# Kernel optimization log

Hardware: AMD Instinct MI355X
Metric: run time of the kernel (lower is better)

## Reference

```python
import jax, jax.numpy as jnp
import numpy as np

B, L, G, D = 4096, 64, 8, 128
N_ITEMS, N_USERS, N_RATINGS = 100000, 50000, 5


def setup_inputs() -> dict:
    key = jax.random.key(0)
    ks = jax.random.split(key, 16)
    s = jnp.float32(0.02)
    return dict(
        nodes=jax.random.randint(ks[0], (B, G), 0, N_USERS),
        history_u=jax.random.randint(ks[1], (B, L), 0, N_ITEMS),
        history_r=jax.random.randint(ks[2], (B, L), 0, N_RATINGS),
        hist_len=jax.random.randint(ks[3], (B,), 0, L),
        v2e_weight=jax.random.normal(ks[4], (N_ITEMS, D), dtype=jnp.float32) * s,
        u2e_weight=jax.random.normal(ks[5], (N_USERS, D), dtype=jnp.float32) * s,
        r2e_weight=jax.random.normal(ks[6], (N_RATINGS, D), dtype=jnp.float32) * s,
        W1=jax.random.normal(ks[7], (2 * D, D), dtype=jnp.float32) * s,
        b1=jnp.zeros((D,), jnp.float32),
        W2=jax.random.normal(ks[8], (D, D), dtype=jnp.float32) * s,
        b2=jnp.zeros((D,), jnp.float32),
        att1_W=jax.random.normal(ks[9], (2 * D, D), dtype=jnp.float32) * s,
        att1_b=jnp.zeros((D,), jnp.float32),
        att2_W=jax.random.normal(ks[10], (D, D), dtype=jnp.float32) * s,
        att2_b=jnp.zeros((D,), jnp.float32),
        att3_W=jax.random.normal(ks[11], (D, 1), dtype=jnp.float32) * s,
        att3_b=jnp.zeros((1,), jnp.float32),
        ge_W=jax.random.normal(ks[12], (D, D), dtype=jnp.float32) * s,
        ge_b=jnp.zeros((D,), jnp.float32),
    )


def reference(nodes, history_u, history_r, hist_len,
              v2e_weight, u2e_weight, r2e_weight,
              W1, b1, W2, b2,
              att1_W, att1_b, att2_W, att2_b, att3_W, att3_b,
              ge_W, ge_b):
    lengths = hist_len + 1                      # ensure >=1 valid history entry per group
    e_uv = v2e_weight[history_u]                # [B, L, D] item-history gather
    e_r = r2e_weight[history_r]                 # [B, L, D] rating gather
    members = u2e_weight[nodes]                 # [B, G, D] member gather
    # Group_Embedding: pool members to one rep per group
    g = jax.nn.relu(members.mean(axis=1) @ ge_W + ge_b)            # [B, D]
    # per-history 2-layer MLP (w_r1, w_r2)
    x = jax.nn.relu(jnp.concatenate([e_uv, e_r], axis=-1) @ W1 + b1)
    o = jax.nn.relu(x @ W2 + b2)                # [B, L, D] o_history
    # Attention: cat(o_history, group_rep) -> relu -> relu -> scalar, softmax over L
    g_rep = jnp.broadcast_to(g[:, None, :], o.shape)               # [B, L, D]
    a = jax.nn.relu(jnp.concatenate([o, g_rep], axis=-1) @ att1_W + att1_b)
    a = jax.nn.relu(a @ att2_W + att2_b)
    logits = (a @ att3_W + att3_b)[..., 0]      # [B, L]
    mask = jnp.arange(L)[None, :] < lengths[:, None]
    logits = jnp.where(mask, logits, jnp.float32(-1e9))
    att = jax.nn.softmax(logits, axis=-1) * mask                   # ragged masked softmax
    # torch.mm(o_history.t(), att_w).t() == attention-weighted reduce over L
    return jnp.einsum('bl,bld->bd', att, o)     # [B, D]
```

## Files before the change

### kernel.cpp

```cpp
#include <hip/hip_runtime.h>
#include <hip/hip_bf16.h>

#define DD 128
#define TILE_BYTES 32768
#define WS_R_OFF   196608
#define WS_GB_OFF  199168

typedef __attribute__((ext_vector_type(8))) short bf16x8;
typedef __attribute__((ext_vector_type(4))) float f32x4;

__device__ inline unsigned short f2bf(float f) {
  unsigned u = __float_as_uint(f);
  return (unsigned short)((u + 0x7fffu + ((u >> 16) & 1u)) >> 16);
}

__device__ inline void async16(void* ldsp, const void* gp) {
  __builtin_amdgcn_global_load_lds(
      (const __attribute__((address_space(1))) void*)gp,
      (__attribute__((address_space(3))) void*)ldsp, 16, 0, 0);
}

__device__ inline void fill_w(char* slot, const char* src, int tid) {
  int w = tid >> 6, lane = tid & 63;
  #pragma unroll
  for (int i = 0; i < 8; ++i) {
    int ofs = ((i << 2) + w) << 10;
    async16(slot + ofs, src + ofs + lane * 16);
  }
}

__device__ inline bf16x8 ldfrag(const char* buf, int rowbase, int kk, int lane) {
  int row = rowbase + (lane & 15);
  int off = (row << 8) + (kk << 6) + (lane & 48);
  off ^= (row & 7) << 4;
  return *(const bf16x8*)(buf + off);
}

__device__ inline bf16x8 ldAg(const float* rp, int kk, int lane) {
  const float4* p = (const float4*)(rp + (kk << 5) + ((lane >> 4) << 3));
  float4 f0 = p[0], f1 = p[1];
  bf16x8 r;
  r[0] = (short)f2bf(f0.x); r[1] = (short)f2bf(f0.y);
  r[2] = (short)f2bf(f0.z); r[3] = (short)f2bf(f0.w);
  r[4] = (short)f2bf(f1.x); r[5] = (short)f2bf(f1.y);
  r[6] = (short)f2bf(f1.z); r[7] = (short)f2bf(f1.w);
  return r;
}

__device__ inline uint2 pack4(float v0, float v1, float v2, float v3) {
  return make_uint2((unsigned)f2bf(v0) | ((unsigned)f2bf(v1) << 16),
                    (unsigned)f2bf(v2) | ((unsigned)f2bf(v3) << 16));
}

#define MFMA(a, b, c) __builtin_amdgcn_mfma_f32_16x16x32_bf16((a), (b), (c), 0, 0, 0)

__global__ __launch_bounds__(256) void prep_weights(
    const float* __restrict__ W1, const float* __restrict__ W2,
    const float* __restrict__ a1W, const float* __restrict__ a2W,
    const float* __restrict__ geW,
    const float* __restrict__ r2e, const float* __restrict__ b1,
    unsigned short* __restrict__ wsw, float* __restrict__ Rp) {
  int gid = blockIdx.x * 256 + threadIdx.x;
  if (gid < 12288) {
    int tile = gid >> 11, idx = gid & 2047;
    int row = idx >> 4, slot = idx & 15;
    int slot2 = slot ^ (row & 7);
    const float* W; int kb;
    switch (tile) {
      case 0:  W = W1;  kb = 0;   break;
      case 1:  W = W2;  kb = 0;   break;
      case 2:  W = a1W; kb = 0;   break;
      case 3:  W = a2W; kb = 0;   break;
      case 4:  W = geW; kb = 0;   break;
      default: W = a1W; kb = 128; break;
    }
    unsigned pk[4];
    #pragma unroll
    for (int p = 0; p < 4; ++p) {
      unsigned short lo = f2bf(W[(size_t)(kb + slot2 * 8 + 2 * p) * DD + row]);
      unsigned short hi = f2bf(W[(size_t)(kb + slot2 * 8 + 2 * p + 1) * DD + row]);
      pk[p] = (unsigned)lo | ((unsigned)hi << 16);
    }
    *(uint4*)(wsw + (size_t)tile * 16384 + (size_t)idx * 8) =
        make_uint4(pk[0], pk[1], pk[2], pk[3]);
  } else {
    int t = gid - 12288;
    for (int idx = t; idx < 640; idx += 256) {
      int r = idx >> 7, d = idx & 127;
      float s = b1[d];
      for (int k = 0; k < 128; ++k)
        s = fmaf(r2e[r * DD + k], W1[(size_t)(DD + k) * DD + d], s);
      Rp[idx] = s;
    }
  }
}

__global__ __launch_bounds__(256, 2) void prep_gb(
    const int* __restrict__ nodes, const float* __restrict__ u2e,
    const float* __restrict__ geb, const float* __restrict__ a1b,
    const char* __restrict__ tiles, float* __restrict__ gbv) {
  __shared__ char mean_s[4096];
  __shared__ char g_s[4096];
  __shared__ char wslot[32768];
  __shared__ int nodes_s[128];
  int tid = threadIdx.x, w = tid >> 6, lane = tid & 63;
  int b0 = blockIdx.x * 16;
  if (tid < 128) nodes_s[tid] = nodes[b0 * 8 + tid];
  fill_w(wslot, tiles + 4 * TILE_BYTES, tid);
  __syncthreads();
  for (int idx = tid; idx < 2048; idx += 256) {
    int row = idx >> 7, d = idx & 127;
    float m = 0.f;
    #pragma unroll
    for (int j = 0; j < 8; ++j)
      m += u2e[(size_t)nodes_s[row * 8 + j] * DD + d];
    m *= 0.125f;
    int off = ((row << 8) + (d << 1)) ^ ((row & 7) << 4);
    *(unsigned short*)(mean_s + off) = f2bf(m);
  }
  __syncthreads();
  int cb = lane & 15, rb = (lane >> 4) << 2;
  f32x4 acc[2] = {(f32x4)(0.f), (f32x4)(0.f)};
  #pragma unroll
  for (int kk = 0; kk < 4; ++kk) {
    bf16x8 a = ldfrag(mean_s, 0, kk, lane);
    #pragma unroll
    for (int nf = 0; nf < 2; ++nf) {
      bf16x8 b = ldfrag(wslot, w * 32 + nf * 16, kk, lane);
      acc[nf] = MFMA(a, b, acc[nf]);
    }
  }
  __syncthreads();
  fill_w(wslot, tiles + 5 * TILE_BYTES, tid);
  #pragma unroll
  for (int nf = 0; nf < 2; ++nf) {
    int col = w * 32 + nf * 16 + cb;
    float gb2 = geb[col];
    #pragma unroll
    for (int j = 0; j < 4; ++j) {
      int row = rb + j;
      float v = fmaxf(acc[nf][j] + gb2, 0.f);
      int off = ((row << 8) + (col << 1)) ^ ((row & 7) << 4);
      *(unsigned short*)(g_s + off) = f2bf(v);
    }
  }
  __syncthreads();
  acc[0] = (f32x4)(0.f); acc[1] = (f32x4)(0.f);
  #pragma unroll
  for (int kk = 0; kk < 4; ++kk) {
    bf16x8 a = ldfrag(g_s, 0, kk, lane);
    #pragma unroll
    for (int nf = 0; nf < 2; ++nf) {
      bf16x8 b = ldfrag(wslot, w * 32 + nf * 16, kk, lane);
      acc[nf] = MFMA(a, b, acc[nf]);
    }
  }
  #pragma unroll
  for (int nf = 0; nf < 2; ++nf) {
    int col = w * 32 + nf * 16 + cb;
    float bb = a1b[col];
    #pragma unroll
    for (int j = 0; j < 4; ++j)
      gbv[(size_t)(b0 + rb + j) * DD + col] = acc[nf][j] + bb;
  }
}

__device__ inline void gemmWX(f32x4 acc[8], const char* Wt, const char* Xt,
                              int mfw, int nlw, int lane) {
  #pragma unroll
  for (int kk = 0; kk < 4; ++kk) {
    bf16x8 bf0 = ldfrag(Xt, nlw * 32, kk, lane);
    bf16x8 bf1 = ldfrag(Xt, nlw * 32 + 16, kk, lane);
    #pragma unroll
    for (int mf = 0; mf < 4; ++mf) {
      bf16x8 a = ldfrag(Wt, mfw * 64 + mf * 16, kk, lane);
      acc[mf * 2]     = MFMA(a, bf0, acc[mf * 2]);
      acc[mf * 2 + 1] = MFMA(a, bf1, acc[mf * 2 + 1]);
    }
  }
}

__global__ __launch_bounds__(256, 3) void main_kernel(
    const int* __restrict__ hu, const int* __restrict__ hr,
    const int* __restrict__ hlen,
    const float* __restrict__ v2e,
    const float* __restrict__ b2, const float* __restrict__ a2b,
    const float* __restrict__ a3W, const float* __restrict__ a3b,
    const char* __restrict__ tiles, const float* __restrict__ Rp,
    const float* __restrict__ gbv, float* __restrict__ out) {
  __shared__ char W[32768];
  __shared__ char X[16384];
  __shared__ float lpart[2][64];
  __shared__ float att_s[64];
  __shared__ float red_s[2][128];

  const int tid = threadIdx.x, lane = tid & 63;
  const int wv = tid >> 6;
  const int mfw = wv >> 1, nlw = wv & 1;
  const int cb = lane & 15, g = lane >> 4;
  const int b0 = blockIdx.x;

  fill_w(W, tiles, tid);
  const int l0 = nlw * 32 + cb, l1 = l0 + 16;
  const int hu0 = hu[b0 * 64 + l0], hu1 = hu[b0 * 64 + l1];
  const int hr0 = hr[b0 * 64 + l0], hr1 = hr[b0 * 64 + l1];
  __syncthreads();

  f32x4 acc[8];
  #pragma unroll
  for (int i = 0; i < 8; ++i) acc[i] = (f32x4)(0.f);

  {
    const float* rp0 = v2e + (size_t)hu0 * DD;
    const float* rp1 = v2e + (size_t)hu1 * DD;
    #pragma unroll
    for (int kk = 0; kk < 4; ++kk) {
      bf16x8 bf0 = ldAg(rp0, kk, lane);
      bf16x8 bf1 = ldAg(rp1, kk, lane);
      #pragma unroll
      for (int mf = 0; mf < 4; ++mf) {
        bf16x8 a = ldfrag(W, mfw * 64 + mf * 16, kk, lane);
        acc[mf * 2]     = MFMA(a, bf0, acc[mf * 2]);
        acc[mf * 2 + 1] = MFMA(a, bf1, acc[mf * 2 + 1]);
      }
    }
  }
  __syncthreads();
  fill_w(W, tiles + TILE_BYTES, tid);
  #pragma unroll
  for (int mf = 0; mf < 4; ++mf) {
    int f0 = mfw * 64 + mf * 16 + g * 4;
    float4 r0 = *(const float4*)(Rp + hr0 * DD + f0);
    float4 r1 = *(const float4*)(Rp + hr1 * DD + f0);
    f32x4 v0 = acc[mf * 2], v1 = acc[mf * 2 + 1];
    uint2 p0 = pack4(fmaxf(v0[0] + r0.x, 0.f), fmaxf(v0[1] + r0.y, 0.f),
                     fmaxf(v0[2] + r0.z, 0.f), fmaxf(v0[3] + r0.w, 0.f));
    uint2 p1 = pack4(fmaxf(v1[0] + r1.x, 0.f), fmaxf(v1[1] + r1.y, 0.f),
                     fmaxf(v1[2] + r1.z, 0.f), fmaxf(v1[3] + r1.w, 0.f));
    int o0 = ((l0 << 8) + (f0 << 1)) ^ ((l0 & 7) << 4);
    int o1 = ((l1 << 8) + (f0 << 1)) ^ ((l1 & 7) << 4);
    *(uint2*)(X + o0) = p0;
    *(uint2*)(X + o1) = p1;
  }
  __syncthreads();

  #pragma unroll
  for (int i = 0; i < 8; ++i) acc[i] = (f32x4)(0.f);
  gemmWX(acc, W, X, mfw, nlw, lane);
  __syncthreads();
  fill_w(W, tiles + 2 * TILE_BYTES, tid);
  uint2 opk[8];
  #pragma unroll
  for (int mf = 0; mf < 4; ++mf) {
    int f0 = mfw * 64 + mf * 16 + g * 4;
    float4 bb = *(const float4*)(b2 + f0);
    f32x4 v0 = acc[mf * 2], v1 = acc[mf * 2 + 1];
    uint2 p0 = pack4(fmaxf(v0[0] + bb.x, 0.f), fmaxf(v0[1] + bb.y, 0.f),
                     fmaxf(v0[2] + bb.z, 0.f), fmaxf(v0[3] + bb.w, 0.f));
    uint2 p1 = pack4(fmaxf(v1[0] + bb.x, 0.f), fmaxf(v1[1] + bb.y, 0.f),
                     fmaxf(v1[2] + bb.z, 0.f), fmaxf(v1[3] + bb.w, 0.f));
    opk[mf * 2] = p0; opk[mf * 2 + 1] = p1;
    int o0 = ((l0 << 8) + (f0 << 1)) ^ ((l0 & 7) << 4);
    int o1 = ((l1 << 8) + (f0 << 1)) ^ ((l1 & 7) << 4);
    *(uint2*)(X + o0) = p0;
    *(uint2*)(X + o1) = p1;
  }
  __syncthreads();

  #pragma unroll
  for (int i = 0; i < 8; ++i) acc[i] = (f32x4)(0.f);
  gemmWX(acc, W, X, mfw, nlw, lane);
  __syncthreads();
  fill_w(W, tiles + 3 * TILE_BYTES, tid);
  #pragma unroll
  for (int mf = 0; mf < 4; ++mf) {
    int f0 = mfw * 64 + mf * 16 + g * 4;
    float4 gg = *(const float4*)(gbv + (size_t)b0 * DD + f0);
    f32x4 v0 = acc[mf * 2], v1 = acc[mf * 2 + 1];
    uint2 p0 = pack4(fmaxf(v0[0] + gg.x, 0.f), fmaxf(v0[1] + gg.y, 0.f),
                     fmaxf(v0[2] + gg.z, 0.f), fmaxf(v0[3] + gg.w, 0.f));
    uint2 p1 = pack4(fmaxf(v1[0] + gg.x, 0.f), fmaxf(v1[1] + gg.y, 0.f),
                     fmaxf(v1[2] + gg.z, 0.f), fmaxf(v1[3] + gg.w, 0.f));
    int o0 = ((l0 << 8) + (f0 << 1)) ^ ((l0 & 7) << 4);
    int o1 = ((l1 << 8) + (f0 << 1)) ^ ((l1 & 7) << 4);
    *(uint2*)(X + o0) = p0;
    *(uint2*)(X + o1) = p1;
  }
  __syncthreads();

  #pragma unroll
  for (int i = 0; i < 8; ++i) acc[i] = (f32x4)(0.f);
  gemmWX(acc, W, X, mfw, nlw, lane);
  {
    float s0 = 0.f, s1 = 0.f;
    #pragma unroll
    for (int mf = 0; mf < 4; ++mf) {
      int f0 = mfw * 64 + mf * 16 + g * 4;
      float4 ab = *(const float4*)(a2b + f0);
      float4 aw = *(const float4*)(a3W + f0);
      f32x4 v0 = acc[mf * 2], v1 = acc[mf * 2 + 1];
      s0 = fmaf(fmaxf(v0[0] + ab.x, 0.f), aw.x, s0);
      s0 = fmaf(fmaxf(v0[1] + ab.y, 0.f), aw.y, s0);
      s0 = fmaf(fmaxf(v0[2] + ab.z, 0.f), aw.z, s0);
      s0 = fmaf(fmaxf(v0[3] + ab.w, 0.f), aw.w, s0);
      s1 = fmaf(fmaxf(v1[0] + ab.x, 0.f), aw.x, s1);
      s1 = fmaf(fmaxf(v1[1] + ab.y, 0.f), aw.y, s1);
      s1 = fmaf(fmaxf(v1[2] + ab.z, 0.f), aw.z, s1);
      s1 = fmaf(fmaxf(v1[3] + ab.w, 0.f), aw.w, s1);
    }
    s0 += __shfl_xor(s0, 16); s0 += __shfl_xor(s0, 32);
    s1 += __shfl_xor(s1, 16); s1 += __shfl_xor(s1, 32);
    if (g == 0) { lpart[mfw][l0] = s0; lpart[mfw][l1] = s1; }
  }
  __syncthreads();

  if (tid < 64) {
    float lv = lpart[0][tid] + lpart[1][tid] + a3b[0];
    int len = hlen[b0] + 1;
    bool valid = tid < len;
    if (!valid) lv = -1e30f;
    float m = lv;
    #pragma unroll
    for (int off = 32; off; off >>= 1) m = fmaxf(m, __shfl_xor(m, off));
    float pe = valid ? expf(lv - m) : 0.f;
    float s = pe;
    #pragma unroll
    for (int off = 32; off; off >>= 1) s += __shfl_xor(s, off);
    att_s[tid] = pe / s;
  }
  __syncthreads();

  {
    float att0 = att_s[l0], att1 = att_s[l1];
    float p[4][4];
    #pragma unroll
    for (int mf = 0; mf < 4; ++mf) {
      uint2 q0 = opk[mf * 2], q1 = opk[mf * 2 + 1];
      p[mf][0] = att0 * __uint_as_float(q0.x << 16)
               + att1 * __uint_as_float(q1.x << 16);
      p[mf][1] = att0 * __uint_as_float(q0.x & 0xffff0000u)
               + att1 * __uint_as_float(q1.x & 0xffff0000u);
      p[mf][2] = att0 * __uint_as_float(q0.y << 16)
               + att1 * __uint_as_float(q1.y << 16);
      p[mf][3] = att0 * __uint_as_float(q0.y & 0xffff0000u)
               + att1 * __uint_as_float(q1.y & 0xffff0000u);
    }
    #pragma unroll
    for (int m = 1; m < 16; m <<= 1) {
      #pragma unroll
      for (int mf = 0; mf < 4; ++mf) {
        p[mf][0] += __shfl_xor(p[mf][0], m);
        p[mf][1] += __shfl_xor(p[mf][1], m);
        p[mf][2] += __shfl_xor(p[mf][2], m);
        p[mf][3] += __shfl_xor(p[mf][3], m);
      }
    }
    if (cb == 0) {
      #pragma unroll
      for (int mf = 0; mf < 4; ++mf) {
        int d = mfw * 64 + mf * 16 + g * 4;
        red_s[nlw][d + 0] = p[mf][0];
        red_s[nlw][d + 1] = p[mf][1];
        red_s[nlw][d + 2] = p[mf][2];
        red_s[nlw][d + 3] = p[mf][3];
      }
    }
  }
  __syncthreads();
  if (tid < 128)
    out[(size_t)b0 * DD + tid] = red_s[0][tid] + red_s[1][tid];
}

extern "C" void kernel_launch(void* const* d_in, const int* in_sizes, int n_in,
                              void* d_out, int out_size, void* d_ws, size_t ws_size,
                              hipStream_t stream) {
  const int*   nodes = (const int*)d_in[0];
  const int*   hu    = (const int*)d_in[1];
  const int*   hr    = (const int*)d_in[2];
  const int*   hlen  = (const int*)d_in[3];
  const float* v2e   = (const float*)d_in[4];
  const float* u2e   = (const float*)d_in[5];
  const float* r2e   = (const float*)d_in[6];
  const float* W1    = (const float*)d_in[7];
  const float* b1    = (const float*)d_in[8];
  const float* W2    = (const float*)d_in[9];
  const float* b2    = (const float*)d_in[10];
  const float* a1W   = (const float*)d_in[11];
  const float* a1b   = (const float*)d_in[12];
  const float* a2W   = (const float*)d_in[13];
  const float* a2b   = (const float*)d_in[14];
  const float* a3W   = (const float*)d_in[15];
  const float* a3b   = (const float*)d_in[16];
  const float* geW   = (const float*)d_in[17];
  const float* geb   = (const float*)d_in[18];
  float* out = (float*)d_out;

  unsigned short* wsw = (unsigned short*)d_ws;
  const char* tiles = (const char*)d_ws;
  float* Rp  = (float*)((char*)d_ws + WS_R_OFF);
  float* gbv = (float*)((char*)d_ws + WS_GB_OFF);

  prep_weights<<<49, 256, 0, stream>>>(W1, W2, a1W, a2W, geW, r2e, b1, wsw, Rp);
  prep_gb<<<256, 256, 0, stream>>>(nodes, u2e, geb, a1b, tiles, gbv);
  main_kernel<<<4096, 256, 0, stream>>>(
      hu, hr, hlen, v2e, b2, a2b, a3W, a3b, tiles, Rp, gbv, out);
}
```

Measured before the change: 111.2 us.

## Make main kernel persistent with resident weights, two rows per iteration

```diff
diff --git a/kernel.cpp b/kernel.cpp
--- a/kernel.cpp
+++ b/kernel.cpp
@@ -180,7 +180,7 @@
   }
 }
 
-__global__ __launch_bounds__(256, 3) void main_kernel(
+__global__ __launch_bounds__(512, 2) void main_kernel(
     const int* __restrict__ hu, const int* __restrict__ hr,
     const int* __restrict__ hlen,
     const float* __restrict__ v2e,
@@ -188,187 +188,262 @@
     const float* __restrict__ a3W, const float* __restrict__ a3b,
     const char* __restrict__ tiles, const float* __restrict__ Rp,
     const float* __restrict__ gbv, float* __restrict__ out) {
-  __shared__ char W[32768];
-  __shared__ char X[16384];
-  __shared__ float lpart[2][64];
-  __shared__ float att_s[64];
-  __shared__ float red_s[2][128];
+  __shared__ char smem[133760];
+  char*  W1s = smem;
+  char*  W2s = smem + 32768;
+  char*  A1s = smem + 65536;
+  char*  XA  = smem + 98304;
+  char*  XB  = smem + 114688;
+  float* Rs  = (float*)(smem + 131072);
 
   const int tid = threadIdx.x, lane = tid & 63;
   const int wv = tid >> 6;
-  const int mfw = wv >> 1, nlw = wv & 1;
+  const int rowsel = wv >> 2;
+  const int w4 = wv & 3;
+  const int mfw = w4 >> 1, nlw = w4 & 1;
   const int cb = lane & 15, g = lane >> 4;
-  const int b0 = blockIdx.x;
-
-  fill_w(W, tiles, tid);
+  char* X = rowsel ? XB : XA;
+
+  #pragma unroll
+  for (int i = 0; i < 4; ++i) {
+    int ofs = (i * 8 + wv) << 10;
+    async16(W1s + ofs, tiles + ofs + lane * 16);
+    async16(W2s + ofs, tiles + TILE_BYTES + ofs + lane * 16);
+    async16(A1s + ofs, tiles + 2 * TILE_BYTES + ofs + lane * 16);
+  }
+  for (int i = tid; i < 640; i += 512)
+    Rs[(i >> 7) * 132 + (i & 127)] = Rp[i];
+
+  bf16x8 a2Wr[16];
+  {
+    const char* a2g = tiles + 3 * TILE_BYTES;
+    #pragma unroll
+    for (int mf = 0; mf < 4; ++mf)
+      #pragma unroll
+      for (int kk = 0; kk < 4; ++kk) {
+        int row = mfw * 64 + mf * 16 + cb;
+        int off = ((row << 8) + (kk << 6) + (lane & 48)) ^ ((row & 7) << 4);
+        a2Wr[mf * 4 + kk] = *(const bf16x8*)(a2g + off);
+      }
+  }
+  float4 a2br[4], a3wr[4];
+  #pragma unroll
+  for (int mf = 0; mf < 4; ++mf) {
+    int f0 = mfw * 64 + mf * 16 + g * 4;
+    a2br[mf] = *(const float4*)(a2b + f0);
+    a3wr[mf] = *(const float4*)(a3W + f0);
+  }
+  const float a3bv = a3b[0];
+
   const int l0 = nlw * 32 + cb, l1 = l0 + 16;
-  const int hu0 = hu[b0 * 64 + l0], hu1 = hu[b0 * 64 + l1];
-  const int hr0 = hr[b0 * 64 + l0], hr1 = hr[b0 * 64 + l1];
+  const int rbase = blockIdx.x * 8;
+  int r = rbase + rowsel;
+  int hu0 = hu[r * 64 + l0], hu1 = hu[r * 64 + l1];
+  int hr0 = hr[r * 64 + l0], hr1 = hr[r * 64 + l1];
   __syncthreads();
 
-  f32x4 acc[8];
-  #pragma unroll
-  for (int i = 0; i < 8; ++i) acc[i] = (f32x4)(0.f);
-
-  {
-    const float* rp0 = v2e + (size_t)hu0 * DD;
-    const float* rp1 = v2e + (size_t)hu1 * DD;
+  for (int p = 0; p < 4; ++p) {
+    f32x4 acc[8];
+    #pragma unroll
+    for (int i = 0; i < 8; ++i) acc[i] = (f32x4)(0.f);
+
+    {
+      const float* rp0 = v2e + (size_t)hu0 * DD;
+      const float* rp1 = v2e + (size_t)hu1 * DD;
+      #pragma unroll
+      for (int kk = 0; kk < 4; ++kk) {
+        bf16x8 bf0 = ldAg(rp0, kk, lane);
+        bf16x8 bf1 = ldAg(rp1, kk, lane);
+        #pragma unroll
+        for (int mf = 0; mf < 4; ++mf) {
+          bf16x8 a = ldfrag(W1s, mfw * 64 + mf * 16, kk, lane);
+          acc[mf * 2]     = MFMA(a, bf0, acc[mf * 2]);
+          acc[mf * 2 + 1] = MFMA(a, bf1, acc[mf * 2 + 1]);
+        }
+      }
+    }
+    #pragma unroll
+    for (int mf = 0; mf < 4; ++mf) {
+      int f0 = mfw * 64 + mf * 16 + g * 4;
+      float4 r0 = *(const float4*)(Rs + hr0 * 132 + f0);
+      float4 r1 = *(const float4*)(Rs + hr1 * 132 + f0);
+      f32x4 v0 = acc[mf * 2], v1 = acc[mf * 2 + 1];
+      uint2 p0 = pack4(fmaxf(v0[0] + r0.x, 0.f), fmaxf(v0[1] + r0.y, 0.f),
+                       fmaxf(v0[2] + r0.z, 0.f), fmaxf(v0[3] + r0.w, 0.f));
+      uint2 p1 = pack4(fmaxf(v1[0] + r1.x, 0.f), fmaxf(v1[1] + r1.y, 0.f),
+                       fmaxf(v1[2] + r1.z, 0.f), fmaxf(v1[3] + r1.w, 0.f));
+      int o0 = ((l0 << 8) + (f0 << 1)) ^ ((l0 & 7) << 4);
+      int o1 = ((l1 << 8) + (f0 << 1)) ^ ((l1 & 7) << 4);
+      *(uint2*)(X + o0) = p0;
+      *(uint2*)(X + o1) = p1;
+    }
+    __syncthreads();
+
+    float4 b2v[4];
+    #pragma unroll
+    for (int mf = 0; mf < 4; ++mf)
+      b2v[mf] = *(const float4*)(b2 + mfw * 64 + mf * 16 + g * 4);
+
+    #pragma unroll
+    for (int i = 0; i < 8; ++i) acc[i] = (f32x4)(0.f);
+    gemmWX(acc, W2s, X, mfw, nlw, lane);
+    __syncthreads();
+    uint2 opk[8];
+    #pragma unroll
+    for (int mf = 0; mf < 4; ++mf) {
+      int f0 = mfw * 64 + mf * 16 + g * 4;
+      float4 bb = b2v[mf];
+      f32x4 v0 = acc[mf * 2], v1 = acc[mf * 2 + 1];
+      uint2 p0 = pack4(fmaxf(v0[0] + bb.x, 0.f), fmaxf(v0[1] + bb.y, 0.f),
+                       fmaxf(v0[2] + bb.z, 0.f), fmaxf(v0[3] + bb.w, 0.f));
+      uint2 p1 = pack4(fmaxf(v1[0] + bb.x, 0.f), fmaxf(v1[1] + bb.y, 0.f),
+                       fmaxf(v1[2] + bb.z, 0.f), fmaxf(v1[3] + bb.w, 0.f));
+      opk[mf * 2] = p0; opk[mf * 2 + 1] = p1;
+      int o0 = ((l0 << 8) + (f0 << 1)) ^ ((l0 & 7) << 4);
+      int o1 = ((l1 << 8) + (f0 << 1)) ^ ((l1 & 7) << 4);
+      *(uint2*)(X + o0) = p0;
+      *(uint2*)(X + o1) = p1;
+    }
+    __syncthreads();
+
+    float4 gg[4];
+    #pragma unroll
+    for (int mf = 0; mf < 4; ++mf)
+      gg[mf] = *(const float4*)(gbv + (size_t)r * DD + mfw * 64 + mf * 16 + g * 4);
+
+    #pragma unroll
+    for (int i = 0; i < 8; ++i) acc[i] = (f32x4)(0.f);
+    gemmWX(acc, A1s, X, mfw, nlw, lane);
+    __syncthreads();
+    #pragma unroll
+    for (int mf = 0; mf < 4; ++mf) {
+      int f0 = mfw * 64 + mf * 16 + g * 4;
+      float4 gv = gg[mf];
+      f32x4 v0 = acc[mf * 2], v1 = acc[mf * 2 + 1];
+      uint2 p0 = pack4(fmaxf(v0[0] + gv.x, 0.f), fmaxf(v0[1] + gv.y, 0.f),
+                       fmaxf(v0[2] + gv.z, 0.f), fmaxf(v0[3] + gv.w, 0.f));
+      uint2 p1 = pack4(fmaxf(v1[0] + gv.x, 0.f), fmaxf(v1[1] + gv.y, 0.f),
+                       fmaxf(v1[2] + gv.z, 0.f), fmaxf(v1[3] + gv.w, 0.f));
+      int o0 = ((l0 << 8) + (f0 << 1)) ^ ((l0 & 7) << 4);
+      int o1 = ((l1 << 8) + (f0 << 1)) ^ ((l1 & 7) << 4);
+      *(uint2*)(X + o0) = p0;
+      *(uint2*)(X + o1) = p1;
+    }
+    __syncthreads();
+
+    int hu0n = 0, hu1n = 0, hr0n = 0, hr1n = 0;
+    if (p < 3) {
+      int rn = r + 2;
+      hu0n = hu[rn * 64 + l0]; hu1n = hu[rn * 64 + l1];
+      hr0n = hr[rn * 64 + l0]; hr1n = hr[rn * 64 + l1];
+    }
+
+    #pragma unroll
+    for (int i = 0; i < 8; ++i) acc[i] = (f32x4)(0.f);
     #pragma unroll
     for (int kk = 0; kk < 4; ++kk) {
-      bf16x8 bf0 = ldAg(rp0, kk, lane);
-      bf16x8 bf1 = ldAg(rp1, kk, lane);
+      bf16x8 bf0 = ldfrag(X, nlw * 32, kk, lane);
+      bf16x8 bf1 = ldfrag(X, nlw * 32 + 16, kk, lane);
       #pragma unroll
       for (int mf = 0; mf < 4; ++mf) {
-        bf16x8 a = ldfrag(W, mfw * 64 + mf * 16, kk, lane);
+        bf16x8 a = a2Wr[mf * 4 + kk];
         acc[mf * 2]     = MFMA(a, bf0, acc[mf * 2]);
         acc[mf * 2 + 1] = MFMA(a, bf1, acc[mf * 2 + 1]);
       }
     }
-  }
-  __syncthreads();
-  fill_w(W, tiles + TILE_BYTES, tid);
-  #pragma unroll
-  for (int mf = 0; mf < 4; ++mf) {
-    int f0 = mfw * 64 + mf * 16 + g * 4;
-    float4 r0 = *(const float4*)(Rp + hr0 * DD + f0);
-    float4 r1 = *(const float4*)(Rp + hr1 * DD + f0);
-    f32x4 v0 = acc[mf * 2], v1 = acc[mf * 2 + 1];
-    uint2 p0 = pack4(fmaxf(v0[0] + r0.x, 0.f), fmaxf(v0[1] + r0.y, 0.f),
-                     fmaxf(v0[2] + r0.z, 0.f), fmaxf(v0[3] + r0.w, 0.f));
-    uint2 p1 = pack4(fmaxf(v1[0] + r1.x, 0.f), fmaxf(v1[1] + r1.y, 0.f),
-                     fmaxf(v1[2] + r1.z, 0.f), fmaxf(v1[3] + r1.w, 0.f));
-    int o0 = ((l0 << 8) + (f0 << 1)) ^ ((l0 & 7) << 4);
-    int o1 = ((l1 << 8) + (f0 << 1)) ^ ((l1 & 7) << 4);
-    *(uint2*)(X + o0) = p0;
-    *(uint2*)(X + o1) = p1;
-  }
-  __syncthreads();
-
-  #pragma unroll
-  for (int i = 0; i < 8; ++i) acc[i] = (f32x4)(0.f);
-  gemmWX(acc, W, X, mfw, nlw, lane);
-  __syncthreads();
-  fill_w(W, tiles + 2 * TILE_BYTES, tid);
-  uint2 opk[8];
-  #pragma unroll
-  for (int mf = 0; mf < 4; ++mf) {
-    int f0 = mfw * 64 + mf * 16 + g * 4;
-    float4 bb = *(const float4*)(b2 + f0);
-    f32x4 v0 = acc[mf * 2], v1 = acc[mf * 2 + 1];
-    uint2 p0 = pack4(fmaxf(v0[0] + bb.x, 0.f), fmaxf(v0[1] + bb.y, 0.f),
-                     fmaxf(v0[2] + bb.z, 0.f), fmaxf(v0[3] + bb.w, 0.f));
-    uint2 p1 = pack4(fmaxf(v1[0] + bb.x, 0.f), fmaxf(v1[1] + bb.y, 0.f),
-                     fmaxf(v1[2] + bb.z, 0.f), fmaxf(v1[3] + bb.w, 0.f));
-    opk[mf * 2] = p0; opk[mf * 2 + 1] = p1;
-    int o0 = ((l0 << 8) + (f0 << 1)) ^ ((l0 & 7) << 4);
-    int o1 = ((l1 << 8) + (f0 << 1)) ^ ((l1 & 7) << 4);
-    *(uint2*)(X + o0) = p0;
-    *(uint2*)(X + o1) = p1;
-  }
-  __syncthreads();
-
-  #pragma unroll
-  for (int i = 0; i < 8; ++i) acc[i] = (f32x4)(0.f);
-  gemmWX(acc, W, X, mfw, nlw, lane);
-  __syncthreads();
-  fill_w(W, tiles + 3 * TILE_BYTES, tid);
-  #pragma unroll
-  for (int mf = 0; mf < 4; ++mf) {
-    int f0 = mfw * 64 + mf * 16 + g * 4;
-    float4 gg = *(const float4*)(gbv + (size_t)b0 * DD + f0);
-    f32x4 v0 = acc[mf * 2], v1 = acc[mf * 2 + 1];
-    uint2 p0 = pack4(fmaxf(v0[0] + gg.x, 0.f), fmaxf(v0[1] + gg.y, 0.f),
-                     fmaxf(v0[2] + gg.z, 0.f), fmaxf(v0[3] + gg.w, 0.f));
-    uint2 p1 = pack4(fmaxf(v1[0] + gg.x, 0.f), fmaxf(v1[1] + gg.y, 0.f),
-                     fmaxf(v1[2] + gg.z, 0.f), fmaxf(v1[3] + gg.w, 0.f));
-    int o0 = ((l0 << 8) + (f0 << 1)) ^ ((l0 & 7) << 4);
-    int o1 = ((l1 << 8) + (f0 << 1)) ^ ((l1 & 7) << 4);
-    *(uint2*)(X + o0) = p0;
-    *(uint2*)(X + o1) = p1;
-  }
-  __syncthreads();
-
-  #pragma unroll
-  for (int i = 0; i < 8; ++i) acc[i] = (f32x4)(0.f);
-  gemmWX(acc, W, X, mfw, nlw, lane);
-  {
-    float s0 = 0.f, s1 = 0.f;
-    #pragma unroll
-    for (int mf = 0; mf < 4; ++mf) {
-      int f0 = mfw * 64 + mf * 16 + g * 4;
-      float4 ab = *(const float4*)(a2b + f0);
-      float4 aw = *(const float4*)(a3W + f0);
-      f32x4 v0 = acc[mf * 2], v1 = acc[mf * 2 + 1];
-      s0 = fmaf(fmaxf(v0[0] + ab.x, 0.f), aw.x, s0);
-      s0 = fmaf(fmaxf(v0[1] + ab.y, 0.f), aw.y, s0);
-      s0 = fmaf(fmaxf(v0[2] + ab.z, 0.f), aw.z, s0);
-      s0 = fmaf(fmaxf(v0[3] + ab.w, 0.f), aw.w, s0);
-      s1 = fmaf(fmaxf(v1[0] + ab.x, 0.f), aw.x, s1);
-      s1 = fmaf(fmaxf(v1[1] + ab.y, 0.f), aw.y, s1);
-      s1 = fmaf(fmaxf(v1[2] + ab.z, 0.f), aw.z, s1);
-      s1 = fmaf(fmaxf(v1[3] + ab.w, 0.f), aw.w, s1);
-    }
-    s0 += __shfl_xor(s0, 16); s0 += __shfl_xor(s0, 32);
-    s1 += __shfl_xor(s1, 16); s1 += __shfl_xor(s1, 32);
-    if (g == 0) { lpart[mfw][l0] = s0; lpart[mfw][l1] = s1; }
-  }
-  __syncthreads();
-
-  if (tid < 64) {
-    float lv = lpart[0][tid] + lpart[1][tid] + a3b[0];
-    int len = hlen[b0] + 1;
-    bool valid = tid < len;
-    if (!valid) lv = -1e30f;
-    float m = lv;
-    #pragma unroll
-    for (int off = 32; off; off >>= 1) m = fmaxf(m, __shfl_xor(m, off));
-    float pe = valid ? expf(lv - m) : 0.f;
-    float s = pe;
-    #pragma unroll
-    for (int off = 32; off; off >>= 1) s += __shfl_xor(s, off);
-    att_s[tid] = pe / s;
-  }
-  __syncthreads();
-
-  {
-    float att0 = att_s[l0], att1 = att_s[l1];
-    float p[4][4];
-    #pragma unroll
-    for (int mf = 0; mf < 4; ++mf) {
-      uint2 q0 = opk[mf * 2], q1 = opk[mf * 2 + 1];
-      p[mf][0] = att0 * __uint_as_float(q0.x << 16)
-               + att1 * __uint_as_float(q1.x << 16);
-      p[mf][1] = att0 * __uint_as_float(q0.x & 0xffff0000u)
-               + att1 * __uint_as_float(q1.x & 0xffff0000u);
-      p[mf][2] = att0 * __uint_as_float(q0.y << 16)
-               + att1 * __uint_as_float(q1.y << 16);
-      p[mf][3] = att0 * __uint_as_float(q0.y & 0xffff0000u)
-               + att1 * __uint_as_float(q1.y & 0xffff0000u);
-    }
-    #pragma unroll
-    for (int m = 1; m < 16; m <<= 1) {
+    __syncthreads();
+
+    {
+      float s0 = 0.f, s1 = 0.f;
       #pragma unroll
       for (int mf = 0; mf < 4; ++mf) {
-        p[mf][0] += __shfl_xor(p[mf][0], m);
-        p[mf][1] += __shfl_xor(p[mf][1], m);
-        p[mf][2] += __shfl_xor(p[mf][2], m);
-        p[mf][3] += __shfl_xor(p[mf][3], m);
-      }
-    }
-    if (cb == 0) {
+        float4 ab = a2br[mf], aw = a3wr[mf];
+        f32x4 v0 = acc[mf * 2], v1 = acc[mf * 2 + 1];
+        s0 = fmaf(fmaxf(v0[0] + ab.x, 0.f), aw.x, s0);
+        s0 = fmaf(fmaxf(v0[1] + ab.y, 0.f), aw.y, s0);
+        s0 = fmaf(fmaxf(v0[2] + ab.z, 0.f), aw.z, s0);
+        s0 = fmaf(fmaxf(v0[3] + ab.w, 0.f), aw.w, s0);
+        s1 = fmaf(fmaxf(v1[0] + ab.x, 0.f), aw.x, s1);
+        s1 = fmaf(fmaxf(v1[1] + ab.y, 0.f), aw.y, s1);
+        s1 = fmaf(fmaxf(v1[2] + ab.z, 0.f), aw.z, s1);
+        s1 = fmaf(fmaxf(v1[3] + ab.w, 0.f), aw.w, s1);
+      }
+      s0 += __shfl_xor(s0, 16); s0 += __shfl_xor(s0, 32);
+      s1 += __shfl_xor(s1, 16); s1 += __shfl_xor(s1, 32);
+      if (g == 0) {
+        *(float*)(X + mfw * 256 + l0 * 4) = s0;
+        *(float*)(X + mfw * 256 + l1 * 4) = s1;
+      }
+    }
+    __syncthreads();
+
+    if (w4 == 0) {
+      int l = lane;
+      float lv = *(const float*)(X + l * 4) + *(const float*)(X + 256 + l * 4) + a3bv;
+      int len = hlen[r] + 1;
+      bool valid = l < len;
+      if (!valid) lv = -1e30f;
+      float m = lv;
+      #pragma unroll
+      for (int off = 32; off; off >>= 1) m = fmaxf(m, __shfl_xor(m, off));
+      float pe = valid ? expf(lv - m) : 0.f;
+      float s = pe;
+      #pragma unroll
+      for (int off = 32; off; off >>= 1) s += __shfl_xor(s, off);
+      *(float*)(X + 512 + l * 4) = pe / s;
+    }
+    __syncthreads();
+
+    {
+      float att0 = *(const float*)(X + 512 + l0 * 4);
+      float att1 = *(const float*)(X + 512 + l1 * 4);
+      float pr[4][4];
       #pragma unroll
       for (int mf = 0; mf < 4; ++mf) {
-        int d = mfw * 64 + mf * 16 + g * 4;
-        red_s[nlw][d + 0] = p[mf][0];
-        red_s[nlw][d + 1] = p[mf][1];
-        red_s[nlw][d + 2] = p[mf][2];
-        red_s[nlw][d + 3] = p[mf][3];
-      }
-    }
-  }
-  __syncthreads();
-  if (tid < 128)
-    out[(size_t)b0 * DD + tid] = red_s[0][tid] + red_s[1][tid];
+        uint2 q0 = opk[mf * 2], q1 = opk[mf * 2 + 1];
+        pr[mf][0] = att0 * __uint_as_float(q0.x << 16)
+                  + att1 * __uint_as_float(q1.x << 16);
+        pr[mf][1] = att0 * __uint_as_float(q0.x & 0xffff0000u)
+                  + att1 * __uint_as_float(q1.x & 0xffff0000u);
+        pr[mf][2] = att0 * __uint_as_float(q0.y << 16)
+                  + att1 * __uint_as_float(q1.y << 16);
+        pr[mf][3] = att0 * __uint_as_float(q0.y & 0xffff0000u)
+                  + att1 * __uint_as_float(q1.y & 0xffff0000u);
+      }
+      #pragma unroll
+      for (int m = 1; m < 16; m <<= 1) {
+        #pragma unroll
+        for (int mf = 0; mf < 4; ++mf) {
+          pr[mf][0] += __shfl_xor(pr[mf][0], m);
+          pr[mf][1] += __shfl_xor(pr[mf][1], m);
+          pr[mf][2] += __shfl_xor(pr[mf][2], m);
+          pr[mf][3] += __shfl_xor(pr[mf][3], m);
+        }
+      }
+      if (cb == 0) {
+        #pragma unroll
+        for (int mf = 0; mf < 4; ++mf) {
+          int f0 = mfw * 64 + mf * 16 + g * 4;
+          float* rd = (float*)(X + 1024 + nlw * 512);
+          rd[f0 + 0] = pr[mf][0];
+          rd[f0 + 1] = pr[mf][1];
+          rd[f0 + 2] = pr[mf][2];
+          rd[f0 + 3] = pr[mf][3];
+        }
+      }
+    }
+    __syncthreads();
+
+    if (tid < 128 || (tid >= 256 && tid < 384)) {
+      int d = tid & 127;
+      out[(size_t)r * DD + d] = *(const float*)(X + 1024 + d * 4)
+                              + *(const float*)(X + 1536 + d * 4);
+    }
+    __syncthreads();
+
+    hu0 = hu0n; hu1 = hu1n; hr0 = hr0n; hr1 = hr1n;
+    r += 2;
+  }
 }
 
 extern "C" void kernel_launch(void* const* d_in, const int* in_sizes, int n_in,
@@ -402,6 +477,6 @@
 
   prep_weights<<<49, 256, 0, stream>>>(W1, W2, a1W, a2W, geW, r2e, b1, wsw, Rp);
   prep_gb<<<256, 256, 0, stream>>>(nodes, u2e, geb, a1b, tiles, gbv);
-  main_kernel<<<4096, 256, 0, stream>>>(
+  main_kernel<<<512, 512, 0, stream>>>(
       hu, hr, hlen, v2e, b2, a2b, a3W, a3b, tiles, Rp, gbv, out);
 }
```

Measured after the change: 157.6 us. 1.42x slower.

## Read weight fragments directly from global memory and use hardware bf16 pack conversion

Applied to the files above, without the earlier changes.

```diff
diff --git a/kernel.cpp b/kernel.cpp
--- a/kernel.cpp
+++ b/kernel.cpp
@@ -12,6 +12,17 @@
 __device__ inline unsigned short f2bf(float f) {
   unsigned u = __float_as_uint(f);
   return (unsigned short)((u + 0x7fffu + ((u >> 16) & 1u)) >> 16);
+}
+__device__ inline float bf2f_lo(unsigned v) { return __uint_as_float(v << 16); }
+__device__ inline float bf2f_hi(unsigned v) { return __uint_as_float(v & 0xffff0000u); }
+
+__device__ inline unsigned cvtpk(float lo, float hi) {
+  unsigned r;
+  asm("v_cvt_pk_bf16_f32 %0, %1, %2" : "=v"(r) : "v"(lo), "v"(hi));
+  return r;
+}
+__device__ inline uint2 pack4(float v0, float v1, float v2, float v3) {
+  return make_uint2(cvtpk(v0, v1), cvtpk(v2, v3));
 }
 
 __device__ inline void async16(void* ldsp, const void* gp) {
@@ -36,20 +47,19 @@
   return *(const bf16x8*)(buf + off);
 }
 
+__device__ inline bf16x8 ldfragG(const char* gbuf, int rowbase, int kk, int lane) {
+  int row = rowbase + (lane & 15);
+  int off = (row << 8) + (kk << 6) + (lane & 48);
+  off ^= (row & 7) << 4;
+  return *(const bf16x8*)(gbuf + off);
+}
+
 __device__ inline bf16x8 ldAg(const float* rp, int kk, int lane) {
   const float4* p = (const float4*)(rp + (kk << 5) + ((lane >> 4) << 3));
   float4 f0 = p[0], f1 = p[1];
-  bf16x8 r;
-  r[0] = (short)f2bf(f0.x); r[1] = (short)f2bf(f0.y);
-  r[2] = (short)f2bf(f0.z); r[3] = (short)f2bf(f0.w);
-  r[4] = (short)f2bf(f1.x); r[5] = (short)f2bf(f1.y);
-  r[6] = (short)f2bf(f1.z); r[7] = (short)f2bf(f1.w);
-  return r;
-}
-
-__device__ inline uint2 pack4(float v0, float v1, float v2, float v3) {
-  return make_uint2((unsigned)f2bf(v0) | ((unsigned)f2bf(v1) << 16),
-                    (unsigned)f2bf(v2) | ((unsigned)f2bf(v3) << 16));
+  uint4 u = make_uint4(cvtpk(f0.x, f0.y), cvtpk(f0.z, f0.w),
+                       cvtpk(f1.x, f1.y), cvtpk(f1.z, f1.w));
+  return __builtin_bit_cast(bf16x8, u);
 }
 
 #define MFMA(a, b, c) __builtin_amdgcn_mfma_f32_16x16x32_bf16((a), (b), (c), 0, 0, 0)
@@ -165,22 +175,22 @@
   }
 }
 
-__device__ inline void gemmWX(f32x4 acc[8], const char* Wt, const char* Xt,
-                              int mfw, int nlw, int lane) {
+__device__ inline void gemmG(f32x4 acc[8], const char* Wg, const char* Xt,
+                             int mfw, int nlw, int lane) {
   #pragma unroll
   for (int kk = 0; kk < 4; ++kk) {
     bf16x8 bf0 = ldfrag(Xt, nlw * 32, kk, lane);
     bf16x8 bf1 = ldfrag(Xt, nlw * 32 + 16, kk, lane);
     #pragma unroll
     for (int mf = 0; mf < 4; ++mf) {
-      bf16x8 a = ldfrag(Wt, mfw * 64 + mf * 16, kk, lane);
+      bf16x8 a = ldfragG(Wg, mfw * 64 + mf * 16, kk, lane);
       acc[mf * 2]     = MFMA(a, bf0, acc[mf * 2]);
       acc[mf * 2 + 1] = MFMA(a, bf1, acc[mf * 2 + 1]);
     }
   }
 }
 
-__global__ __launch_bounds__(256, 3) void main_kernel(
+__global__ __launch_bounds__(256, 4) void main_kernel(
     const int* __restrict__ hu, const int* __restrict__ hr,
     const int* __restrict__ hlen,
     const float* __restrict__ v2e,
@@ -188,7 +198,6 @@
     const float* __restrict__ a3W, const float* __restrict__ a3b,
     const char* __restrict__ tiles, const float* __restrict__ Rp,
     const float* __restrict__ gbv, float* __restrict__ out) {
-  __shared__ char W[32768];
   __shared__ char X[16384];
   __shared__ float lpart[2][64];
   __shared__ float att_s[64];
@@ -199,12 +208,14 @@
   const int mfw = wv >> 1, nlw = wv & 1;
   const int cb = lane & 15, g = lane >> 4;
   const int b0 = blockIdx.x;
-
-  fill_w(W, tiles, tid);
+  const char* W1g = tiles;
+  const char* W2g = tiles + TILE_BYTES;
+  const char* A1g = tiles + 2 * TILE_BYTES;
+  const char* A2g = tiles + 3 * TILE_BYTES;
+
   const int l0 = nlw * 32 + cb, l1 = l0 + 16;
   const int hu0 = hu[b0 * 64 + l0], hu1 = hu[b0 * 64 + l1];
   const int hr0 = hr[b0 * 64 + l0], hr1 = hr[b0 * 64 + l1];
-  __syncthreads();
 
   f32x4 acc[8];
   #pragma unroll
@@ -219,14 +230,12 @@
       bf16x8 bf1 = ldAg(rp1, kk, lane);
       #pragma unroll
       for (int mf = 0; mf < 4; ++mf) {
-        bf16x8 a = ldfrag(W, mfw * 64 + mf * 16, kk, lane);
+        bf16x8 a = ldfragG(W1g, mfw * 64 + mf * 16, kk, lane);
         acc[mf * 2]     = MFMA(a, bf0, acc[mf * 2]);
         acc[mf * 2 + 1] = MFMA(a, bf1, acc[mf * 2 + 1]);
       }
     }
   }
-  __syncthreads();
-  fill_w(W, tiles + TILE_BYTES, tid);
   #pragma unroll
   for (int mf = 0; mf < 4; ++mf) {
     int f0 = mfw * 64 + mf * 16 + g * 4;
@@ -246,9 +255,8 @@
 
   #pragma unroll
   for (int i = 0; i < 8; ++i) acc[i] = (f32x4)(0.f);
-  gemmWX(acc, W, X, mfw, nlw, lane);
-  __syncthreads();
-  fill_w(W, tiles + 2 * TILE_BYTES, tid);
+  gemmG(acc, W2g, X, mfw, nlw, lane);
+  __syncthreads();
   uint2 opk[8];
   #pragma unroll
   for (int mf = 0; mf < 4; ++mf) {
@@ -269,18 +277,17 @@
 
   #pragma unroll
   for (int i = 0; i < 8; ++i) acc[i] = (f32x4)(0.f);
-  gemmWX(acc, W, X, mfw, nlw, lane);
-  __syncthreads();
-  fill_w(W, tiles + 3 * TILE_BYTES, tid);
+  gemmG(acc, A1g, X, mfw, nlw, lane);
+  __syncthreads();
   #pragma unroll
   for (int mf = 0; mf < 4; ++mf) {
     int f0 = mfw * 64 + mf * 16 + g * 4;
-    float4 gg = *(const float4*)(gbv + (size_t)b0 * DD + f0);
+    float4 gv = *(const float4*)(gbv + (size_t)b0 * DD + f0);
     f32x4 v0 = acc[mf * 2], v1 = acc[mf * 2 + 1];
-    uint2 p0 = pack4(fmaxf(v0[0] + gg.x, 0.f), fmaxf(v0[1] + gg.y, 0.f),
-                     fmaxf(v0[2] + gg.z, 0.f), fmaxf(v0[3] + gg.w, 0.f));
-    uint2 p1 = pack4(fmaxf(v1[0] + gg.x, 0.f), fmaxf(v1[1] + gg.y, 0.f),
-                     fmaxf(v1[2] + gg.z, 0.f), fmaxf(v1[3] + gg.w, 0.f));
+    uint2 p0 = pack4(fmaxf(v0[0] + gv.x, 0.f), fmaxf(v0[1] + gv.y, 0.f),
+                     fmaxf(v0[2] + gv.z, 0.f), fmaxf(v0[3] + gv.w, 0.f));
+    uint2 p1 = pack4(fmaxf(v1[0] + gv.x, 0.f), fmaxf(v1[1] + gv.y, 0.f),
+                     fmaxf(v1[2] + gv.z, 0.f), fmaxf(v1[3] + gv.w, 0.f));
     int o0 = ((l0 << 8) + (f0 << 1)) ^ ((l0 & 7) << 4);
     int o1 = ((l1 << 8) + (f0 << 1)) ^ ((l1 & 7) << 4);
     *(uint2*)(X + o0) = p0;
@@ -290,7 +297,7 @@
 
   #pragma unroll
   for (int i = 0; i < 8; ++i) acc[i] = (f32x4)(0.f);
-  gemmWX(acc, W, X, mfw, nlw, lane);
+  gemmG(acc, A2g, X, mfw, nlw, lane);
   {
     float s0 = 0.f, s1 = 0.f;
     #pragma unroll
@@ -332,41 +339,38 @@
 
   {
     float att0 = att_s[l0], att1 = att_s[l1];
-    float p[4][4];
+    float pr[4][4];
     #pragma unroll
     for (int mf = 0; mf < 4; ++mf) {
       uint2 q0 = opk[mf * 2], q1 = opk[mf * 2 + 1];
-      p[mf][0] = att0 * __uint_as_float(q0.x << 16)
-               + att1 * __uint_as_float(q1.x << 16);
-      p[mf][1] = att0 * __uint_as_float(q0.x & 0xffff0000u)
-               + att1 * __uint_as_float(q1.x & 0xffff0000u);
-      p[mf][2] = att0 * __uint_as_float(q0.y << 16)
-               + att1 * __uint_as_float(q1.y << 16);
-      p[mf][3] = att0 * __uint_as_float(q0.y & 0xffff0000u)
-               + att1 * __uint_as_float(q1.y & 0xffff0000u);
+      pr[mf][0] = att0 * bf2f_lo(q0.x) + att1 * bf2f_lo(q1.x);
+      pr[mf][1] = att0 * bf2f_hi(q0.x) + att1 * bf2f_hi(q1.x);
+      pr[mf][2] = att0 * bf2f_lo(q0.y) + att1 * bf2f_lo(q1.y);
+      pr[mf][3] = att0 * bf2f_hi(q0.y) + att1 * bf2f_hi(q1.y);
     }
     #pragma unroll
     for (int m = 1; m < 16; m <<= 1) {
       #pragma unroll
       for (int mf = 0; mf < 4; ++mf) {
-        p[mf][0] += __shfl_xor(p[mf][0], m);
-        p[mf][1] += __shfl_xor(p[mf][1], m);
-        p[mf][2] += __shfl_xor(p[mf][2], m);
-        p[mf][3] += __shfl_xor(p[mf][3], m);
+        pr[mf][0] += __shfl_xor(pr[mf][0], m);
+        pr[mf][1] += __shfl_xor(pr[mf][1], m);
+        pr[mf][2] += __shfl_xor(pr[mf][2], m);
+        pr[mf][3] += __shfl_xor(pr[mf][3], m);
       }
     }
     if (cb == 0) {
       #pragma unroll
       for (int mf = 0; mf < 4; ++mf) {
-        int d = mfw * 64 + mf * 16 + g * 4;
-        red_s[nlw][d + 0] = p[mf][0];
-        red_s[nlw][d + 1] = p[mf][1];
-        red_s[nlw][d + 2] = p[mf][2];
-        red_s[nlw][d + 3] = p[mf][3];
+        int f0 = mfw * 64 + mf * 16 + g * 4;
+        red_s[nlw][f0 + 0] = pr[mf][0];
+        red_s[nlw][f0 + 1] = pr[mf][1];
+        red_s[nlw][f0 + 2] = pr[mf][2];
+        red_s[nlw][f0 + 3] = pr[mf][3];
       }
     }
   }
   __syncthreads();
+
   if (tid < 128)
     out[(size_t)b0 * DD + tid] = red_s[0][tid] + red_s[1][tid];
 }
```

After: 113.2 us. No clear change (+1.8%).
